# Kernel tuning notes

Measured on AMD Instinct MI355X. Metric: run time of the kernel, lower is better.

## Reference

```python
import jax, jax.numpy as jnp
import numpy as np

TAU = 0.5  # temperature
W_SCALE = 1.0 / np.sqrt(2048.0)  # keep logits in a sane range (like nn.Linear init)


def setup_inputs() -> dict:
    key = jax.random.key(0)
    k1, k2, k3 = jax.random.split(key, 3)
    B, I, O, N = 8192, 2048, 256, 64
    x = jax.random.normal(k1, (B, I), dtype=jnp.float32)
    W = jax.random.normal(k2, (O, N, I), dtype=jnp.float32) * W_SCALE
    b = jnp.zeros((O, N), dtype=jnp.float32)
    grid = jnp.linspace(-1.0, 1.0, N, dtype=jnp.float32)
    # pre-sampled standard Gumbel noise (reparameterized sampling, fixed for determinism)
    u = jax.random.uniform(k3, (B, O, N), dtype=jnp.float32, minval=1e-6, maxval=1.0 - 1e-6)
    gumbel_noise = -jnp.log(-jnp.log(u))
    return {"x": x, "W": W, "b": b, "grid": grid, "gumbel_noise": gumbel_noise}


def reference(x, W, b, grid, gumbel_noise):
    B = x.shape[0]
    O, N, _ = W.shape
    # per-output-feature linears fused into one GEMM; stack(dim=-1) order -> [B, N, O]
    factors = jnp.einsum('bi,oni->bno', x, W) + b.T  # [B, n_bins, out_features]
    # torch .view(B, out_features, n_bins) on the contiguous stacked tensor == reshape
    factors_logits = factors.reshape(B, O, N)
    # gumbel-softmax sampling (soft), then collapse bins onto the value grid
    y = jax.nn.softmax((factors_logits + gumbel_noise) / TAU, axis=-1)  # [B, O, N]
    encoded = jnp.einsum('bon,n->bo', y, grid)  # [B, out_features]
    return (encoded, factors_logits)
```

## Files before the change

kernel.cpp:

```cpp
#include <hip/hip_runtime.h>
#include <hip/hip_bf16.h>
#include <stdint.h>

typedef __bf16 bf16x8 __attribute__((ext_vector_type(8)));
typedef float f32x4 __attribute__((ext_vector_type(4)));
typedef unsigned short u16x8 __attribute__((ext_vector_type(8)));

#define B_ROWS 8192
#define K_DIM  2048
#define O_DIM  256
#define N_BINS 64
#define J_DIM  (O_DIM * N_BINS)
#define NT32   (K_DIM / 32)

__device__ __forceinline__ unsigned short f2bf(float f) {
    union { float f; unsigned u; } v; v.f = f;
    unsigned r = (v.u + 0x7fffu + ((v.u >> 16) & 1u)) >> 16;
    return (unsigned short)r;
}

__global__ void cvt_x_kernel(const float* __restrict__ x, unsigned short* __restrict__ xb) {
    int i = (blockIdx.x * 256 + threadIdx.x) * 4;
    float4 v = *(const float4*)(x + i);
    ushort4 o;
    o.x = f2bf(v.x); o.y = f2bf(v.y); o.z = f2bf(v.z); o.w = f2bf(v.w);
    *(ushort4*)(xb + i) = o;
}

__global__ void cvt_w_kernel(const float* __restrict__ W, unsigned short* __restrict__ vb) {
    int bid = blockIdx.x;
    int p   = bid >> 1;
    int i0  = (bid & 1) * 1024 + threadIdx.x * 4;
    int src = (p & (O_DIM - 1)) * (N_BINS * K_DIM) + (p >> 8) * K_DIM + i0;
    float4 v = *(const float4*)(W + src);
    ushort4 o;
    o.x = f2bf(v.x); o.y = f2bf(v.y); o.z = f2bf(v.z); o.w = f2bf(v.w);
    *(ushort4*)(vb + (size_t)p * K_DIM + i0) = o;
}

__device__ __forceinline__ u16x8 pack8(float4 a, float4 b) {
    u16x8 r;
    r[0] = f2bf(a.x); r[1] = f2bf(a.y); r[2] = f2bf(a.z); r[3] = f2bf(a.w);
    r[4] = f2bf(b.x); r[5] = f2bf(b.y); r[6] = f2bf(b.z); r[7] = f2bf(b.w);
    return r;
}

#define GLDS(gsrc, ldst) \
    __builtin_amdgcn_global_load_lds((const __attribute__((address_space(1))) void*)(gsrc), \
                                     (__attribute__((address_space(3))) void*)(ldst), 16, 0, 0)
#define SBAR()   __builtin_amdgcn_s_barrier()
#define SCHED0() __builtin_amdgcn_sched_barrier(0)
#define WAIT_VM(N)   do { asm volatile("s_waitcnt vmcnt(" #N ")" ::: "memory"); } while (0)
#define WAIT_LGKM(N) do { asm volatile("s_waitcnt lgkmcnt(" #N ")" ::: "memory"); SCHED0(); } while (0)
#define MFMA(a, b, c) (c) = __builtin_amdgcn_mfma_f32_16x16x32_bf16((a), (b), (c), 0, 0, 0)

#define KTILE_BODY(BUF, STAGE_A, STAGE_B) do {                                          \
    bf16x8 a0_[4], a1_[4], bf_[4];                                                      \
    _Pragma("unroll") for (int m_ = 0; m_ < 4; ++m_)                                    \
        a0_[m_] = *(const bf16x8*)&As[BUF][arb + m_ * 16][slot];                        \
    _Pragma("unroll") for (int n_ = 0; n_ < 4; ++n_)                                    \
        bf_[n_] = *(const bf16x8*)&Bs[BUF][brb + n_ * 16][slot];                        \
    _Pragma("unroll") for (int m_ = 0; m_ < 4; ++m_)                                    \
        a1_[m_] = *(const bf16x8*)&As[BUF][arb + 64 + m_ * 16][slot];                   \
    STAGE_A;                                                                            \
    WAIT_LGKM(4);                                                                       \
    __builtin_amdgcn_s_setprio(1);                                                      \
    _Pragma("unroll") for (int m_ = 0; m_ < 4; ++m_) {                                  \
        MFMA(a0_[m_], bf_[0], acc[m_][0]); MFMA(a0_[m_], bf_[1], acc[m_][1]);           \
        MFMA(a0_[m_], bf_[2], acc[m_][2]); MFMA(a0_[m_], bf_[3], acc[m_][3]);           \
    }                                                                                   \
    __builtin_amdgcn_s_setprio(0);                                                      \
    STAGE_B;                                                                            \
    WAIT_LGKM(0);                                                                       \
    __builtin_amdgcn_s_setprio(1);                                                      \
    _Pragma("unroll") for (int m_ = 0; m_ < 4; ++m_) {                                  \
        MFMA(a1_[m_], bf_[0], acc[4 + m_][0]); MFMA(a1_[m_], bf_[1], acc[4 + m_][1]);   \
        MFMA(a1_[m_], bf_[2], acc[4 + m_][2]); MFMA(a1_[m_], bf_[3], acc[4 + m_][3]);   \
    }                                                                                   \
    __builtin_amdgcn_s_setprio(0);                                                      \
} while (0)

__global__ __launch_bounds__(512, 2) void gemm8_kernel(
    const unsigned short* __restrict__ xb,
    const unsigned short* __restrict__ vb,
    const float* __restrict__ bias,
    float* __restrict__ logits)
{
    __shared__ unsigned short As[4][256][32];
    __shared__ unsigned short Bs[4][256][32];

    const int tid  = threadIdx.x;
    const int lane = tid & 63;
    const int wv   = tid >> 6;
    const int wr   = wv >> 2;
    const int wc   = wv & 3;

    const int bid = blockIdx.x;
    const int swz  = (bid & 7) * 256 + (bid >> 3);
    const int bm   = (swz >> 8) * 4 + (swz & 3);
    const int bn   = (swz & 255) >> 2;
    const int row0 = bm * 256;
    const int col0 = bn * 256;

    const int oss = (tid * 16) ^ (tid & 32);
    const int sr  = oss >> 6;
    const int sc  = (oss >> 1) & 31;

    const unsigned short* gA = xb + (size_t)(row0 + sr) * K_DIM + sc;
    const unsigned short* gB = vb + (size_t)(col0 + sr) * K_DIM + sc;

    auto stageA = [&](int k, int b) {
        const unsigned short* g = gA + k * 32;
        unsigned short* l = &As[b][0][0] + wv * 512;
        GLDS(g, l);
        GLDS(g + (size_t)128 * K_DIM, l + 4096);
    };
    auto stageB = [&](int k, int b) {
        const unsigned short* g = gB + k * 32;
        unsigned short* l = &Bs[b][0][0] + wv * 512;
        GLDS(g, l);
        GLDS(g + (size_t)128 * K_DIM, l + 4096);
    };

    const int arb  = wr * 128 + (lane & 15);
    const int brb  = wc * 64 + (lane & 15);
    const int slot = ((lane >> 4) * 8) ^ ((lane & 8) << 1);

    f32x4 acc[8][4];
#pragma unroll
    for (int m = 0; m < 8; ++m)
#pragma unroll
        for (int n = 0; n < 4; ++n)
            acc[m][n] = (f32x4){0.f, 0.f, 0.f, 0.f};

    stageA(0, 0); stageB(0, 0);
    stageA(1, 1); stageB(1, 1);
    stageA(2, 2); stageB(2, 2);

    for (int it = 0; it < 15; ++it) {
        const int kt0 = it * 4;
#pragma unroll
        for (int u = 0; u < 4; ++u) {
            WAIT_VM(8); SBAR();
            KTILE_BODY(u, stageA(kt0 + u + 3, (u + 3) & 3), stageB(kt0 + u + 3, (u + 3) & 3));
        }
    }
    WAIT_VM(8); SBAR(); KTILE_BODY(0, stageA(63, 3), stageB(63, 3));
    WAIT_VM(8); SBAR(); KTILE_BODY(1, (void)0, (void)0);
    WAIT_VM(4); SBAR(); KTILE_BODY(2, (void)0, (void)0);
    WAIT_VM(0); SBAR(); KTILE_BODY(3, (void)0, (void)0);

    const int r_base = row0 + wr * 128 + (lane >> 4) * 4;
    const int c_base = col0 + wc * 64 + (lane & 15);
#pragma unroll
    for (int n = 0; n < 4; ++n) {
        const int c = c_base + n * 16;
        const float bv = bias[(c & (O_DIM - 1)) * N_BINS + (c >> 8)];
#pragma unroll
        for (int m = 0; m < 8; ++m) {
            const int r = r_base + m * 16;
            float* out = logits + (size_t)r * J_DIM + c;
#pragma unroll
            for (int q = 0; q < 4; ++q)
                out[(size_t)q * J_DIM] = acc[m][n][q] + bv;
        }
    }
}

__global__ __launch_bounds__(256) void gemm_fb(
    const float* __restrict__ xf,
    const float* __restrict__ Wf,
    const float* __restrict__ bias,
    float* __restrict__ logits)
{
    __shared__ unsigned short Asm_[128 * 32];
    __shared__ unsigned short Bsm_[128 * 32];

    const int tid = threadIdx.x;
    const int bid = blockIdx.x;
    const int swz = (bid & 7) * 1024 + (bid >> 3);
    const int row0 = (swz >> 7) * 128;
    const int col0 = (swz & 127) * 128;

    const int lane = tid & 63;
    const int wid  = tid >> 6;
    const int wr   = wid >> 1;
    const int wc   = wid & 1;

    f32x4 acc[4][4];
#pragma unroll
    for (int m = 0; m < 4; ++m)
#pragma unroll
        for (int n = 0; n < 4; ++n)
            acc[m][n] = (f32x4){0.f, 0.f, 0.f, 0.f};

    const int srow = tid >> 2;
    const int koff = (tid & 3) * 8;
    const int ra0 = row0 + srow, ra1 = row0 + 64 + srow;
    const int rb0 = col0 + srow, rb1 = col0 + 64 + srow;

    unsigned short* la0 = &Asm_[tid * 8];
    unsigned short* la1 = &Asm_[(256 + tid) * 8];
    unsigned short* lb0 = &Bsm_[tid * 8];
    unsigned short* lb1 = &Bsm_[(256 + tid) * 8];

    const float* fa0 = xf + (size_t)ra0 * K_DIM + koff;
    const float* fa1 = xf + (size_t)ra1 * K_DIM + koff;
    const float* fb0 = Wf + (size_t)((rb0 & (O_DIM - 1)) * (N_BINS * K_DIM) + (rb0 >> 8) * K_DIM) + koff;
    const float* fb1 = Wf + (size_t)((rb1 & (O_DIM - 1)) * (N_BINS * K_DIM) + (rb1 >> 8) * K_DIM) + koff;

    const int a_row  = wr * 64 + (lane & 15);
    const int b_row  = wc * 64 + (lane & 15);
    const int k_half = (lane >> 4) * 8;

    for (int kt = 0; kt < K_DIM / 32; ++kt) {
        const int kbase = kt * 32;
        *(u16x8*)la0 = pack8(*(const float4*)(fa0 + kbase), *(const float4*)(fa0 + kbase + 4));
        *(u16x8*)la1 = pack8(*(const float4*)(fa1 + kbase), *(const float4*)(fa1 + kbase + 4));
        *(u16x8*)lb0 = pack8(*(const float4*)(fb0 + kbase), *(const float4*)(fb0 + kbase + 4));
        *(u16x8*)lb1 = pack8(*(const float4*)(fb1 + kbase), *(const float4*)(fb1 + kbase + 4));
        __syncthreads();
        bf16x8 af[4], bg[4];
#pragma unroll
        for (int m = 0; m < 4; ++m) af[m] = *(const bf16x8*)&Asm_[(a_row + m * 16) * 32 + k_half];
#pragma unroll
        for (int n = 0; n < 4; ++n) bg[n] = *(const bf16x8*)&Bsm_[(b_row + n * 16) * 32 + k_half];
#pragma unroll
        for (int m = 0; m < 4; ++m)
#pragma unroll
            for (int n = 0; n < 4; ++n)
                MFMA(af[m], bg[n], acc[m][n]);
        __syncthreads();
    }

    const int r_base = row0 + wr * 64 + (lane >> 4) * 4;
    const int c_base = col0 + wc * 64 + (lane & 15);
#pragma unroll
    for (int n = 0; n < 4; ++n) {
        const int c = c_base + n * 16;
        const float bv = bias[(c & (O_DIM - 1)) * N_BINS + (c >> 8)];
#pragma unroll
        for (int m = 0; m < 4; ++m) {
            const int r = r_base + m * 16;
            float* out = logits + (size_t)r * J_DIM + c;
#pragma unroll
            for (int q = 0; q < 4; ++q)
                out[(size_t)q * J_DIM] = acc[m][n][q] + bv;
        }
    }
}

__global__ void softmax_encode_kernel(
    const float* __restrict__ logits,
    const float* __restrict__ gumbel,
    const float* __restrict__ grid,
    float* __restrict__ encoded)
{
    int t = blockIdx.x * 256 + threadIdx.x;
    int g = t >> 4;
    int l = t & 15;
    size_t base = (size_t)g * 64 + l * 4;
    float4 L = *(const float4*)(logits + base);
    float4 G = *(const float4*)(gumbel + base);
    float4 gr = *(const float4*)(grid + l * 4);

    float z0 = (L.x + G.x) * 2.0f;
    float z1 = (L.y + G.y) * 2.0f;
    float z2 = (L.z + G.z) * 2.0f;
    float z3 = (L.w + G.w) * 2.0f;

    float m = fmaxf(fmaxf(z0, z1), fmaxf(z2, z3));
#pragma unroll
    for (int s = 1; s < 16; s <<= 1) m = fmaxf(m, __shfl_xor(m, s, 16));

    float e0 = __expf(z0 - m), e1 = __expf(z1 - m), e2 = __expf(z2 - m), e3 = __expf(z3 - m);
    float ssum = e0 + e1 + e2 + e3;
    float dsum = e0 * gr.x + e1 * gr.y + e2 * gr.z + e3 * gr.w;
#pragma unroll
    for (int s = 1; s < 16; s <<= 1) {
        ssum += __shfl_xor(ssum, s, 16);
        dsum += __shfl_xor(dsum, s, 16);
    }
    if (l == 0) encoded[g] = dsum / ssum;
}

extern "C" void kernel_launch(void* const* d_in, const int* in_sizes, int n_in,
                              void* d_out, int out_size, void* d_ws, size_t ws_size,
                              hipStream_t stream) {
    const float* x      = (const float*)d_in[0];
    const float* W      = (const float*)d_in[1];
    const float* bias   = (const float*)d_in[2];
    const float* grid   = (const float*)d_in[3];
    const float* gumbel = (const float*)d_in[4];

    float* encoded = (float*)d_out;
    float* logits  = (float*)d_out + (size_t)B_ROWS * O_DIM;

    const size_t xb_bytes = (size_t)B_ROWS * K_DIM * 2;
    const size_t vb_bytes = (size_t)J_DIM * K_DIM * 2;

    if (ws_size >= xb_bytes + vb_bytes) {
        unsigned short* xb = (unsigned short*)d_ws;
        unsigned short* vb = (unsigned short*)((char*)d_ws + xb_bytes);
        cvt_x_kernel<<<(B_ROWS * K_DIM) / 1024, 256, 0, stream>>>(x, xb);
        cvt_w_kernel<<<J_DIM * 2, 256, 0, stream>>>(W, vb);
        gemm8_kernel<<<(B_ROWS / 256) * (J_DIM / 256), 512, 0, stream>>>(xb, vb, bias, logits);
    } else {
        gemm_fb<<<(B_ROWS / 128) * (J_DIM / 128), 256, 0, stream>>>(x, W, bias, logits);
    }

    softmax_encode_kernel<<<(B_ROWS * O_DIM * 16) / 256, 256, 0, stream>>>(logits, gumbel, grid, encoded);
}
```

Measured before the change: 836.6 us.

## Double-buffer LDS fragment loads across k-tiles in the GEMM main loop

```diff
diff --git a/kernel.cpp b/kernel.cpp
--- a/kernel.cpp
+++ b/kernel.cpp
@@ -11,7 +11,6 @@
 #define O_DIM  256
 #define N_BINS 64
 #define J_DIM  (O_DIM * N_BINS)
-#define NT32   (K_DIM / 32)
 
 __device__ __forceinline__ unsigned short f2bf(float f) {
     union { float f; unsigned u; } v; v.f = f;
@@ -49,35 +48,35 @@
     __builtin_amdgcn_global_load_lds((const __attribute__((address_space(1))) void*)(gsrc), \
                                      (__attribute__((address_space(3))) void*)(ldst), 16, 0, 0)
 #define SBAR()   __builtin_amdgcn_s_barrier()
-#define SCHED0() __builtin_amdgcn_sched_barrier(0)
-#define WAIT_VM(N)   do { asm volatile("s_waitcnt vmcnt(" #N ")" ::: "memory"); } while (0)
-#define WAIT_LGKM(N) do { asm volatile("s_waitcnt lgkmcnt(" #N ")" ::: "memory"); SCHED0(); } while (0)
+#define WAIT_VM(N) do { asm volatile("s_waitcnt vmcnt(" #N ")" ::: "memory"); } while (0)
 #define MFMA(a, b, c) (c) = __builtin_amdgcn_mfma_f32_16x16x32_bf16((a), (b), (c), 0, 0, 0)
 
-#define KTILE_BODY(BUF, STAGE_A, STAGE_B) do {                                          \
-    bf16x8 a0_[4], a1_[4], bf_[4];                                                      \
+#define ITER_BODY(U, PF, DO_STAGE, STAGE_KT, VMN) do {                                  \
+    constexpr int S_ = (U) & 1;                                                         \
+    constexpr int NU_ = ((U) + 1) & 3;                                                  \
+    if (PF) {                                                                           \
+        _Pragma("unroll") for (int m_ = 0; m_ < 4; ++m_)                                \
+            fa[S_ ^ 1][m_] = *(const bf16x8*)&As[NU_][arb + m_ * 16][slot];             \
+        _Pragma("unroll") for (int n_ = 0; n_ < 4; ++n_)                                \
+            fb[S_ ^ 1][n_] = *(const bf16x8*)&Bs[NU_][brb + n_ * 16][slot];             \
+    }                                                                                   \
     _Pragma("unroll") for (int m_ = 0; m_ < 4; ++m_)                                    \
-        a0_[m_] = *(const bf16x8*)&As[BUF][arb + m_ * 16][slot];                        \
-    _Pragma("unroll") for (int n_ = 0; n_ < 4; ++n_)                                    \
-        bf_[n_] = *(const bf16x8*)&Bs[BUF][brb + n_ * 16][slot];                        \
-    _Pragma("unroll") for (int m_ = 0; m_ < 4; ++m_)                                    \
-        a1_[m_] = *(const bf16x8*)&As[BUF][arb + 64 + m_ * 16][slot];                   \
-    STAGE_A;                                                                            \
-    WAIT_LGKM(4);                                                                       \
+        fa1[m_] = *(const bf16x8*)&As[(U) & 3][arb + 64 + m_ * 16][slot];               \
+    if (DO_STAGE) stageA((STAGE_KT), ((U) + 3) & 3);                                    \
     __builtin_amdgcn_s_setprio(1);                                                      \
     _Pragma("unroll") for (int m_ = 0; m_ < 4; ++m_) {                                  \
-        MFMA(a0_[m_], bf_[0], acc[m_][0]); MFMA(a0_[m_], bf_[1], acc[m_][1]);           \
-        MFMA(a0_[m_], bf_[2], acc[m_][2]); MFMA(a0_[m_], bf_[3], acc[m_][3]);           \
+        MFMA(fa[S_][m_], fb[S_][0], acc[m_][0]); MFMA(fa[S_][m_], fb[S_][1], acc[m_][1]); \
+        MFMA(fa[S_][m_], fb[S_][2], acc[m_][2]); MFMA(fa[S_][m_], fb[S_][3], acc[m_][3]); \
     }                                                                                   \
     __builtin_amdgcn_s_setprio(0);                                                      \
-    STAGE_B;                                                                            \
-    WAIT_LGKM(0);                                                                       \
+    if (DO_STAGE) stageB((STAGE_KT), ((U) + 3) & 3);                                    \
     __builtin_amdgcn_s_setprio(1);                                                      \
     _Pragma("unroll") for (int m_ = 0; m_ < 4; ++m_) {                                  \
-        MFMA(a1_[m_], bf_[0], acc[4 + m_][0]); MFMA(a1_[m_], bf_[1], acc[4 + m_][1]);   \
-        MFMA(a1_[m_], bf_[2], acc[4 + m_][2]); MFMA(a1_[m_], bf_[3], acc[4 + m_][3]);   \
+        MFMA(fa1[m_], fb[S_][0], acc[4 + m_][0]); MFMA(fa1[m_], fb[S_][1], acc[4 + m_][1]); \
+        MFMA(fa1[m_], fb[S_][2], acc[4 + m_][2]); MFMA(fa1[m_], fb[S_][3], acc[4 + m_][3]); \
     }                                                                                   \
     __builtin_amdgcn_s_setprio(0);                                                      \
+    WAIT_VM(VMN); SBAR();                                                               \
 } while (0)
 
 __global__ __launch_bounds__(512, 2) void gemm8_kernel(
@@ -133,22 +132,44 @@
         for (int n = 0; n < 4; ++n)
             acc[m][n] = (f32x4){0.f, 0.f, 0.f, 0.f};
 
+    bf16x8 fa[2][4], fb[2][4], fa1[4];
+
     stageA(0, 0); stageB(0, 0);
     stageA(1, 1); stageB(1, 1);
     stageA(2, 2); stageB(2, 2);
+    WAIT_VM(4); SBAR();
+
+#pragma unroll
+    for (int m = 0; m < 4; ++m) fa[0][m] = *(const bf16x8*)&As[0][arb + m * 16][slot];
+#pragma unroll
+    for (int n = 0; n < 4; ++n) fb[0][n] = *(const bf16x8*)&Bs[0][brb + n * 16][slot];
 
     for (int it = 0; it < 15; ++it) {
         const int kt0 = it * 4;
-#pragma unroll
-        for (int u = 0; u < 4; ++u) {
-            WAIT_VM(8); SBAR();
-            KTILE_BODY(u, stageA(kt0 + u + 3, (u + 3) & 3), stageB(kt0 + u + 3, (u + 3) & 3));
+        ITER_BODY(0, 1, 1, kt0 + 3, 4);
+        ITER_BODY(1, 1, 1, kt0 + 4, 4);
+        ITER_BODY(2, 1, 1, kt0 + 5, 4);
+        ITER_BODY(3, 1, 1, kt0 + 6, 4);
+    }
+    ITER_BODY(0, 1, 1, 63, 4);
+    ITER_BODY(1, 1, 0, 0, 0);
+    ITER_BODY(2, 1, 0, 0, 0);
+    {
+#pragma unroll
+        for (int m = 0; m < 4; ++m) fa1[m] = *(const bf16x8*)&As[3][arb + 64 + m * 16][slot];
+        __builtin_amdgcn_s_setprio(1);
+#pragma unroll
+        for (int m = 0; m < 4; ++m) {
+            MFMA(fa[1][m], fb[1][0], acc[m][0]); MFMA(fa[1][m], fb[1][1], acc[m][1]);
+            MFMA(fa[1][m], fb[1][2], acc[m][2]); MFMA(fa[1][m], fb[1][3], acc[m][3]);
         }
-    }
-    WAIT_VM(8); SBAR(); KTILE_BODY(0, stageA(63, 3), stageB(63, 3));
-    WAIT_VM(8); SBAR(); KTILE_BODY(1, (void)0, (void)0);
-    WAIT_VM(4); SBAR(); KTILE_BODY(2, (void)0, (void)0);
-    WAIT_VM(0); SBAR(); KTILE_BODY(3, (void)0, (void)0);
+#pragma unroll
+        for (int m = 0; m < 4; ++m) {
+            MFMA(fa1[m], fb[1][0], acc[4 + m][0]); MFMA(fa1[m], fb[1][1], acc[4 + m][1]);
+            MFMA(fa1[m], fb[1][2], acc[4 + m][2]); MFMA(fa1[m], fb[1][3], acc[4 + m][3]);
+        }
+        __builtin_amdgcn_s_setprio(0);
+    }
 
     const int r_base = row0 + wr * 128 + (lane >> 4) * 4;
     const int c_base = col0 + wc * 64 + (lane & 15);
```

After: 857.7 us. 2.5% more time.

## Fuse gumbel-softmax and grid encode into GEMM epilogue

Applied to the files above, without the earlier changes.

```diff
diff --git a/kernel.cpp b/kernel.cpp
--- a/kernel.cpp
+++ b/kernel.cpp
@@ -11,7 +11,6 @@
 #define O_DIM  256
 #define N_BINS 64
 #define J_DIM  (O_DIM * N_BINS)
-#define NT32   (K_DIM / 32)
 
 __device__ __forceinline__ unsigned short f2bf(float f) {
     union { float f; unsigned u; } v; v.f = f;
@@ -84,7 +83,10 @@
     const unsigned short* __restrict__ xb,
     const unsigned short* __restrict__ vb,
     const float* __restrict__ bias,
-    float* __restrict__ logits)
+    const float* __restrict__ grid,
+    const float* __restrict__ gumbel,
+    float* __restrict__ logits,
+    float* __restrict__ encoded)
 {
     __shared__ unsigned short As[4][256][32];
     __shared__ unsigned short Bs[4][256][32];
@@ -150,19 +152,51 @@
     WAIT_VM(4); SBAR(); KTILE_BODY(2, (void)0, (void)0);
     WAIT_VM(0); SBAR(); KTILE_BODY(3, (void)0, (void)0);
 
+    const int lane15 = lane & 15;
     const int r_base = row0 + wr * 128 + (lane >> 4) * 4;
-    const int c_base = col0 + wc * 64 + (lane & 15);
+    const int o      = (col0 >> 6) + wc;
+    const int c_base = col0 + wc * 64 + lane15;
+
+    float gridv[4], biasv[4];
 #pragma unroll
     for (int n = 0; n < 4; ++n) {
+        gridv[n] = grid[n * 16 + lane15];
         const int c = c_base + n * 16;
-        const float bv = bias[(c & (O_DIM - 1)) * N_BINS + (c >> 8)];
-#pragma unroll
-        for (int m = 0; m < 8; ++m) {
-            const int r = r_base + m * 16;
-            float* out = logits + (size_t)r * J_DIM + c;
-#pragma unroll
-            for (int q = 0; q < 4; ++q)
-                out[(size_t)q * J_DIM] = acc[m][n][q] + bv;
+        biasv[n] = bias[(c & (O_DIM - 1)) * N_BINS + (c >> 8)];
+    }
+
+#pragma unroll
+    for (int m = 0; m < 8; ++m) {
+#pragma unroll
+        for (int q = 0; q < 4; ++q) {
+            const int r = r_base + m * 16 + q;
+            const size_t rowoff = (size_t)r * J_DIM + c_base;
+            float lg[4], z[4];
+            float gmax = -3.0e38f;
+#pragma unroll
+            for (int n = 0; n < 4; ++n) {
+                lg[n] = acc[m][n][q] + biasv[n];
+                const float gum = gumbel[rowoff + n * 16];
+                z[n] = (lg[n] + gum) * 2.0f;
+                gmax = fmaxf(gmax, z[n]);
+            }
+#pragma unroll
+            for (int n = 0; n < 4; ++n)
+                logits[rowoff + n * 16] = lg[n];
+#pragma unroll
+            for (int s = 1; s < 16; s <<= 1) gmax = fmaxf(gmax, __shfl_xor(gmax, s));
+            float ss = 0.f, ds = 0.f;
+#pragma unroll
+            for (int n = 0; n < 4; ++n) {
+                const float e = __expf(z[n] - gmax);
+                ss += e; ds += e * gridv[n];
+            }
+#pragma unroll
+            for (int s = 1; s < 16; s <<= 1) {
+                ss += __shfl_xor(ss, s);
+                ds += __shfl_xor(ds, s);
+            }
+            if (lane15 == 0) encoded[(size_t)r * O_DIM + o] = ds / ss;
         }
     }
 }
@@ -304,10 +338,10 @@
         unsigned short* vb = (unsigned short*)((char*)d_ws + xb_bytes);
         cvt_x_kernel<<<(B_ROWS * K_DIM) / 1024, 256, 0, stream>>>(x, xb);
         cvt_w_kernel<<<J_DIM * 2, 256, 0, stream>>>(W, vb);
-        gemm8_kernel<<<(B_ROWS / 256) * (J_DIM / 256), 512, 0, stream>>>(xb, vb, bias, logits);
+        gemm8_kernel<<<(B_ROWS / 256) * (J_DIM / 256), 512, 0, stream>>>(
+            xb, vb, bias, grid, gumbel, logits, encoded);
     } else {
         gemm_fb<<<(B_ROWS / 128) * (J_DIM / 128), 256, 0, stream>>>(x, W, bias, logits);
-    }
-
-    softmax_encode_kernel<<<(B_ROWS * O_DIM * 16) / 256, 256, 0, stream>>>(logits, gumbel, grid, encoded);
-}
+        softmax_encode_kernel<<<(B_ROWS * O_DIM * 16) / 256, 256, 0, stream>>>(logits, gumbel, grid, encoded);
+    }
+}
```

Result: no change. 823.3 us (-1.6%).
